# Kernel optimization log

Hardware: AMD Instinct MI355X
Metric: run time of the kernel (lower is better)

Reference implementation:

```python
import jax, jax.numpy as jnp
import numpy as np

N_NODES = 50000

def _gat_layer(x, src, dst, W, a_l, a_r, bias, alpha, agg, act, n_nodes):
    # x: [N, in]; W: [in, H*F]; a_l, a_r: [H, F]; bias: [H*F]
    H, F = a_l.shape
    z = (x @ W).reshape(n_nodes, H, F)                      # [N,H,F]
    el = jnp.einsum('nhf,hf->nh', z, a_l)                   # [N,H]
    er = jnp.einsum('nhf,hf->nh', z, a_r)                   # [N,H]
    e = jax.nn.leaky_relu(el[src] + er[dst], alpha)         # [E,H]
    # segment softmax over in-edges of each destination node
    m = jax.ops.segment_max(e, dst, num_segments=n_nodes)   # [N,H]
    ex = jnp.exp(e - m[dst])                                # [E,H]
    s = jax.ops.segment_sum(ex, dst, num_segments=n_nodes)  # [N,H]
    attn = ex / jnp.maximum(s[dst], 1e-9)                   # [E,H]
    msg = attn[:, :, None] * z[src]                         # [E,H,F]
    h = jax.ops.segment_sum(msg, dst, num_segments=n_nodes) # [N,H,F]
    # identity residual (in_feats == H*F) as in DGL GATConv
    h = h + x.reshape(n_nodes, -1, F)
    h = h + bias.reshape(1, H, F)
    if agg == 'flatten':
        h = h.reshape(n_nodes, H * F)
    else:  # mean over heads
        h = h.mean(axis=1)
    if act is not None:
        h = act(h)
    return h


def setup_inputs() -> dict:
    key = jax.random.key(0)
    ks = jax.random.split(key, 14)
    N, E, D = N_NODES, 800000, 128
    H, F = 4, 32
    sc_in = 1.0 / np.sqrt(D)
    sc_h = 1.0 / np.sqrt(H * F)
    inp = {
        'feats': jax.random.normal(ks[0], (N, D), jnp.float32),
        'src': jax.random.randint(ks[1], (E,), 0, N),
        'dst': jax.random.randint(ks[2], (E,), 0, N),
        'W1': jax.random.normal(ks[3], (D, H * F), jnp.float32) * sc_in,
        'al1': jax.random.normal(ks[4], (H, F), jnp.float32) * sc_h,
        'ar1': jax.random.normal(ks[5], (H, F), jnp.float32) * sc_h,
        'b1': jnp.zeros((H * F,), jnp.float32),
        'W2': jax.random.normal(ks[6], (H * F, H * F), jnp.float32) * sc_h,
        'al2': jax.random.normal(ks[7], (H, F), jnp.float32) * sc_h,
        'ar2': jax.random.normal(ks[8], (H, F), jnp.float32) * sc_h,
        'b2': jnp.zeros((H * F,), jnp.float32),
        'Wp': jax.random.normal(ks[9], (F, 1), jnp.float32) / np.sqrt(F),
        'bp': jnp.zeros((1,), jnp.float32),
    }
    return inp


def reference(feats, src, dst, W1, al1, ar1, b1, W2, al2, ar2, b2, Wp, bp):
    h = _gat_layer(feats, src, dst, W1, al1, ar1, b1, 0.2, 'flatten', jax.nn.elu, N_NODES)
    h = _gat_layer(h, src, dst, W2, al2, ar2, b2, 0.2, 'mean', None, N_NODES)
    return h @ Wp + bp  # [N, 1]
```

## Files before the change

### kernel.cpp

```cpp
#include <hip/hip_runtime.h>
#include <hip/hip_bf16.h>

#define NN 50000
#define NE 800000
#define HF 128
#define MAXDEG 64

#define OFF_FLAG   0u
#define OFF_Z      16668672u
#define OFF_H1     29468672u
#define OFF_EL     42268672u
#define OFF_ER     43068672u
#define OFF_FILL   54000128u
#define OFF_ADJ2   60000000u

typedef __hip_bfloat16 bf16;
typedef unsigned short us16;

#define SCAT_B 3125
#define GEMM_B 782

typedef __attribute__((ext_vector_type(8))) short bf16x8;
typedef __attribute__((ext_vector_type(4))) float f32x4;

__device__ __forceinline__ float us2f(us16 u) {
  union { unsigned int i; float f; } c; c.i = ((unsigned int)u) << 16; return c.f;
}
__device__ __forceinline__ us16 f2us(float f) {
  bf16 h = __float2bfloat16(f);
  union { bf16 h; us16 u; } c; c.h = h; return c.u;
}
__device__ __forceinline__ float blo(unsigned v) {
  union { unsigned i; float f; } c; c.i = v << 16; return c.f;
}
__device__ __forceinline__ float bhi(unsigned v) {
  union { unsigned i; float f; } c; c.i = v & 0xffff0000u; return c.f;
}
__device__ __forceinline__ unsigned pk2(float a, float b) {
  return (unsigned)f2us(a) | ((unsigned)f2us(b) << 16);
}

__device__ __forceinline__ int detect_f32(const us16* __restrict__ u) {
  int t = threadIdx.x;
  int mx = 0;
  for (int i = t; i < 2048; i += 256) {
    int e = (u[i] >> 7) & 0xFF;
    mx = mx > e ? mx : e;
  }
#pragma unroll
  for (int m = 32; m >= 1; m >>= 1) {
    int o = __shfl_xor(mx, m);
    mx = mx > o ? mx : o;
  }
  __shared__ int sred[4];
  if ((t & 63) == 0) sred[t >> 6] = mx;
  __syncthreads();
  int a = sred[0] > sred[1] ? sred[0] : sred[1];
  int b = sred[2] > sred[3] ? sred[2] : sred[3];
  int r = a > b ? a : b;
  return r >= 135;
}

__global__ __launch_bounds__(256) void k_scatter(
    const int* __restrict__ src, const int* __restrict__ dst,
    int* __restrict__ fill, us16* __restrict__ adj2) {
  int e = blockIdx.x * 256 + threadIdx.x;
  int d = dst[e];
  int r = atomicAdd(&fill[d], 1);
  if (r < MAXDEG) adj2[(d << 6) + r] = (us16)src[e];
}

template <int LAYER>
__global__ __launch_bounds__(256) void k_gemm(
    const void* __restrict__ Xv, const void* __restrict__ Wv,
    const void* __restrict__ alr, const void* __restrict__ arr,
    us16* __restrict__ Z, float* __restrict__ el, float* __restrict__ er,
    int* __restrict__ flagp) {
  int tid = threadIdx.x;
  int bx = (int)blockIdx.x;

  __shared__ us16 Wl[HF * HF];
  int f;
  if (LAYER == 1) {
    f = detect_f32((const us16*)Wv);
    if (bx == 0 && tid == 0) *flagp = f;
  } else {
    f = *flagp;
  }

  {
    const float* Wf = (const float*)Wv;
    const us16* Wb = (const us16*)Wv;
    for (int e = tid; e < HF * HF; e += 256) {
      int k = e >> 7, n = e & 127;
      int d = ((((k >> 5) * 8 + (n >> 4)) * 4 + ((k >> 3) & 3)) * 16 + (n & 15)) * 8 + (k & 7);
      Wl[d] = f ? f2us(Wf[e]) : Wb[e];
    }
  }
  __syncthreads();

  int w = tid >> 6;
  int lane = tid & 63;
  int q = lane >> 4;
  int c = lane & 15;
  int m0 = bx * 64 + w * 16;

  int rA = m0 + c;
  if (rA >= NN) rA = NN - 1;
  const us16* xb = (const us16*)Xv + (size_t)rA * HF;
  const float* xf = (const float*)Xv + (size_t)rA * HF;

  f32x4 acc[8] = {};
#pragma unroll
  for (int s = 0; s < 4; ++s) {
    bf16x8 a;
    if (LAYER == 1 && f) {
      float4 v0 = *(const float4*)&xf[s * 32 + q * 8];
      float4 v1 = *(const float4*)&xf[s * 32 + q * 8 + 4];
      union { us16 u[8]; bf16x8 v; } cv;
      cv.u[0] = f2us(v0.x); cv.u[1] = f2us(v0.y);
      cv.u[2] = f2us(v0.z); cv.u[3] = f2us(v0.w);
      cv.u[4] = f2us(v1.x); cv.u[5] = f2us(v1.y);
      cv.u[6] = f2us(v1.z); cv.u[7] = f2us(v1.w);
      a = cv.v;
    } else {
      a = *(const bf16x8*)&xb[s * 32 + q * 8];
    }
#pragma unroll
    for (int t = 0; t < 8; ++t) {
      bf16x8 bb = *(const bf16x8*)&Wl[((((s * 8) + t) * 4 + q) * 16 + c) * 8];
      acc[t] = __builtin_amdgcn_mfma_f32_16x16x32_bf16(a, bb, acc[t], 0, 0, 0);
    }
  }

#pragma unroll
  for (int reg = 0; reg < 4; ++reg) {
    int row = m0 + q * 4 + reg;
    if (row < NN) {
      us16* zrow = Z + (size_t)row * HF;
#pragma unroll
      for (int t = 0; t < 8; ++t) zrow[t * 16 + c] = f2us(acc[t][reg]);
    }
  }

  float alv[8], arv[8];
  {
    const float* alf = (const float*)alr; const us16* alb = (const us16*)alr;
    const float* arf = (const float*)arr; const us16* arb = (const us16*)arr;
#pragma unroll
    for (int t = 0; t < 8; ++t) {
      alv[t] = f ? alf[t * 16 + c] : us2f(alb[t * 16 + c]);
      arv[t] = f ? arf[t * 16 + c] : us2f(arb[t * 16 + c]);
    }
  }
#pragma unroll
  for (int reg = 0; reg < 4; ++reg) {
    int row = m0 + q * 4 + reg;
    float pl[4], pr[4];
#pragma unroll
    for (int h = 0; h < 4; ++h) {
      pl[h] = acc[2 * h][reg] * alv[2 * h] + acc[2 * h + 1][reg] * alv[2 * h + 1];
      pr[h] = acc[2 * h][reg] * arv[2 * h] + acc[2 * h + 1][reg] * arv[2 * h + 1];
    }
#pragma unroll
    for (int m = 1; m < 16; m <<= 1) {
#pragma unroll
      for (int h = 0; h < 4; ++h) {
        pl[h] += __shfl_xor(pl[h], m);
        pr[h] += __shfl_xor(pr[h], m);
      }
    }
    if (row < NN) {
      int cc = c & 3;
      float vl = cc == 0 ? pl[0] : cc == 1 ? pl[1] : cc == 2 ? pl[2] : pl[3];
      float vr = cc == 0 ? pr[0] : cc == 1 ? pr[1] : cc == 2 ? pr[2] : pr[3];
      if (c < 4) el[row * 4 + cc] = vl;
      else if (c < 8) er[row * 4 + cc] = vr;
    }
  }
}

template <int LAYER>
__global__ __launch_bounds__(256) void k_agg(
    const us16* __restrict__ Z, const float* __restrict__ el,
    const float* __restrict__ er, const int* __restrict__ fill,
    const us16* __restrict__ adj2, const void* __restrict__ resid,
    const void* __restrict__ bias, us16* __restrict__ Hout,
    const void* __restrict__ Wp, const void* __restrict__ bp,
    void* __restrict__ out, const int* __restrict__ flag) {
  int f = *flag;
  int n = blockIdx.x * 4 + (threadIdx.x >> 6);
  int lane = threadIdx.x & 63;
  int g = lane >> 4;
  int p = lane & 15;
  int hl = p >> 2;
  int f0 = p * 8;
  int begin = n << 6;

  int sl = (int)adj2[begin + lane];

  int deg = fill[n];
  if (deg > MAXDEG) deg = MAXDEG;
  float erh = er[n * 4 + hl];

  float acc[8] = {};
  float ssum = 0.f;
  for (int k = 0; k * 8 < deg; ++k) {
    int i0 = g + k * 8;
    int i1 = i0 + 4;
    int s0 = __shfl(sl, i0);
    int s1 = __shfl(sl, i1);
    bool v0 = i0 < deg;
    bool v1 = i1 < deg;
    s0 = v0 ? s0 : 0;
    s1 = v1 ? s1 : 0;
    float l0 = el[s0 * 4 + hl];
    float l1 = el[s1 * 4 + hl];
    uint4 za = *(const uint4*)&Z[(size_t)s0 * HF + f0];
    uint4 zb = *(const uint4*)&Z[(size_t)s1 * HF + f0];
    float sc0 = l0 + erh; sc0 = sc0 > 0.f ? sc0 : 0.2f * sc0;
    float sc1 = l1 + erh; sc1 = sc1 > 0.f ? sc1 : 0.2f * sc1;
    float ex0 = v0 ? __expf(sc0) : 0.f;
    float ex1 = v1 ? __expf(sc1) : 0.f;
    ssum += ex0 + ex1;
    acc[0] = fmaf(ex0, blo(za.x), acc[0]); acc[1] = fmaf(ex0, bhi(za.x), acc[1]);
    acc[2] = fmaf(ex0, blo(za.y), acc[2]); acc[3] = fmaf(ex0, bhi(za.y), acc[3]);
    acc[4] = fmaf(ex0, blo(za.z), acc[4]); acc[5] = fmaf(ex0, bhi(za.z), acc[5]);
    acc[6] = fmaf(ex0, blo(za.w), acc[6]); acc[7] = fmaf(ex0, bhi(za.w), acc[7]);
    acc[0] = fmaf(ex1, blo(zb.x), acc[0]); acc[1] = fmaf(ex1, bhi(zb.x), acc[1]);
    acc[2] = fmaf(ex1, blo(zb.y), acc[2]); acc[3] = fmaf(ex1, bhi(zb.y), acc[3]);
    acc[4] = fmaf(ex1, blo(zb.z), acc[4]); acc[5] = fmaf(ex1, bhi(zb.z), acc[5]);
    acc[6] = fmaf(ex1, blo(zb.w), acc[6]); acc[7] = fmaf(ex1, bhi(zb.w), acc[7]);
  }
  ssum += __shfl_xor(ssum, 16); ssum += __shfl_xor(ssum, 32);
#pragma unroll
  for (int j = 0; j < 8; ++j) {
    acc[j] += __shfl_xor(acc[j], 16);
    acc[j] += __shfl_xor(acc[j], 32);
  }
  float inv = 1.f / fmaxf(ssum, 1e-9f);

  float rx[8];
  if (LAYER == 1 && f) {
    const float* rf = (const float*)resid + (size_t)n * HF + f0;
    float4 r0 = *(const float4*)rf;
    float4 r1 = *(const float4*)(rf + 4);
    rx[0] = r0.x; rx[1] = r0.y; rx[2] = r0.z; rx[3] = r0.w;
    rx[4] = r1.x; rx[5] = r1.y; rx[6] = r1.z; rx[7] = r1.w;
  } else {
    uint4 xq = *(const uint4*)((const us16*)resid + (size_t)n * HF + f0);
    rx[0] = blo(xq.x); rx[1] = bhi(xq.x); rx[2] = blo(xq.y); rx[3] = bhi(xq.y);
    rx[4] = blo(xq.z); rx[5] = bhi(xq.z); rx[6] = blo(xq.w); rx[7] = bhi(xq.w);
  }
  float bv[8];
  if (f) {
    const float* bf_ = (const float*)bias + f0;
    bv[0] = bf_[0]; bv[1] = bf_[1]; bv[2] = bf_[2]; bv[3] = bf_[3];
    bv[4] = bf_[4]; bv[5] = bf_[5]; bv[6] = bf_[6]; bv[7] = bf_[7];
  } else {
    uint4 bq = *(const uint4*)((const us16*)bias + f0);
    bv[0] = blo(bq.x); bv[1] = bhi(bq.x); bv[2] = blo(bq.y); bv[3] = bhi(bq.y);
    bv[4] = blo(bq.z); bv[5] = bhi(bq.z); bv[6] = blo(bq.w); bv[7] = bhi(bq.w);
  }
  float t0 = fmaf(acc[0], inv, rx[0] + bv[0]);
  float t1 = fmaf(acc[1], inv, rx[1] + bv[1]);
  float t2 = fmaf(acc[2], inv, rx[2] + bv[2]);
  float t3 = fmaf(acc[3], inv, rx[3] + bv[3]);
  float t4 = fmaf(acc[4], inv, rx[4] + bv[4]);
  float t5 = fmaf(acc[5], inv, rx[5] + bv[5]);
  float t6 = fmaf(acc[6], inv, rx[6] + bv[6]);
  float t7 = fmaf(acc[7], inv, rx[7] + bv[7]);

  if (LAYER == 1) {
    t0 = t0 > 0.f ? t0 : __expf(t0) - 1.f;
    t1 = t1 > 0.f ? t1 : __expf(t1) - 1.f;
    t2 = t2 > 0.f ? t2 : __expf(t2) - 1.f;
    t3 = t3 > 0.f ? t3 : __expf(t3) - 1.f;
    t4 = t4 > 0.f ? t4 : __expf(t4) - 1.f;
    t5 = t5 > 0.f ? t5 : __expf(t5) - 1.f;
    t6 = t6 > 0.f ? t6 : __expf(t6) - 1.f;
    t7 = t7 > 0.f ? t7 : __expf(t7) - 1.f;
    if (g == 0) {
      uint4 o;
      o.x = pk2(t0, t1); o.y = pk2(t2, t3); o.z = pk2(t4, t5); o.w = pk2(t6, t7);
      *(uint4*)&Hout[(size_t)n * HF + f0] = o;
    }
  } else {
    t0 += __shfl_xor(t0, 4); t0 += __shfl_xor(t0, 8);
    t1 += __shfl_xor(t1, 4); t1 += __shfl_xor(t1, 8);
    t2 += __shfl_xor(t2, 4); t2 += __shfl_xor(t2, 8);
    t3 += __shfl_xor(t3, 4); t3 += __shfl_xor(t3, 8);
    t4 += __shfl_xor(t4, 4); t4 += __shfl_xor(t4, 8);
    t5 += __shfl_xor(t5, 4); t5 += __shfl_xor(t5, 8);
    t6 += __shfl_xor(t6, 4); t6 += __shfl_xor(t6, 8);
    t7 += __shfl_xor(t7, 4); t7 += __shfl_xor(t7, 8);
    int fw = (p & 3) * 8;
    float wv0, wv1, wv2, wv3, wv4, wv5, wv6, wv7;
    if (f) {
      const float* wpf = (const float*)Wp;
      wv0 = wpf[fw];     wv1 = wpf[fw + 1]; wv2 = wpf[fw + 2]; wv3 = wpf[fw + 3];
      wv4 = wpf[fw + 4]; wv5 = wpf[fw + 5]; wv6 = wpf[fw + 6]; wv7 = wpf[fw + 7];
    } else {
      const us16* wpb = (const us16*)Wp;
      wv0 = us2f(wpb[fw]);     wv1 = us2f(wpb[fw + 1]);
      wv2 = us2f(wpb[fw + 2]); wv3 = us2f(wpb[fw + 3]);
      wv4 = us2f(wpb[fw + 4]); wv5 = us2f(wpb[fw + 5]);
      wv6 = us2f(wpb[fw + 6]); wv7 = us2f(wpb[fw + 7]);
    }
    float pr = 0.25f * (t0 * wv0 + t1 * wv1 + t2 * wv2 + t3 * wv3 +
                        t4 * wv4 + t5 * wv5 + t6 * wv6 + t7 * wv7);
    pr += __shfl_xor(pr, 1); pr += __shfl_xor(pr, 2);
    if (lane == 0) {
      float bpv = f ? ((const float*)bp)[0] : us2f(((const us16*)bp)[0]);
      float res = pr + bpv;
      if (f) ((float*)out)[n] = res;
      else ((us16*)out)[n] = f2us(res);
    }
  }
}

extern "C" void kernel_launch(void* const* d_in, const int* in_sizes, int n_in,
                              void* d_out, int out_size, void* d_ws, size_t ws_size,
                              hipStream_t stream) {
  const int* src = (const int*)d_in[1];
  const int* dst = (const int*)d_in[2];
  char* ws = (char*)d_ws;
  int* flag   = (int*)(ws + OFF_FLAG);
  us16* z     = (us16*)(ws + OFF_Z);
  us16* h1    = (us16*)(ws + OFF_H1);
  float* el   = (float*)(ws + OFF_EL);
  float* er   = (float*)(ws + OFF_ER);
  int* fill   = (int*)(ws + OFF_FILL);
  us16* adj2  = (us16*)(ws + OFF_ADJ2);

  hipMemsetAsync(fill, 0, (size_t)NN * 4, stream);

  hipLaunchKernelGGL(k_scatter, dim3(SCAT_B), dim3(256), 0, stream,
                     src, dst, fill, adj2);
  hipLaunchKernelGGL((k_gemm<1>), dim3(GEMM_B), dim3(256), 0, stream,
                     d_in[0], d_in[3], d_in[4], d_in[5], z, el, er, flag);
  hipLaunchKernelGGL((k_agg<1>), dim3(NN / 4), dim3(256), 0, stream, z, el, er,
                     fill, adj2, d_in[0], d_in[6], h1,
                     (const void*)nullptr, (const void*)nullptr, (void*)nullptr, flag);
  hipLaunchKernelGGL((k_gemm<2>), dim3(GEMM_B), dim3(256), 0, stream,
                     h1, d_in[7], d_in[8], d_in[9], z, el, er, flag);
  hipLaunchKernelGGL((k_agg<2>), dim3(NN / 4), dim3(256), 0, stream, z, el, er,
                     fill, adj2, h1, d_in[10], (us16*)nullptr,
                     d_in[11], d_in[12], d_out, flag);
}
```

Measured before the change: 268.3 us.

## Pre-swizzle weights and params once in a fused scatter+prep kernel

Folds weight conversion/swizzling for both layers and the small parameter vectors into extra blocks of the edge-scatter kernel, writing bf16 copies to workspace. The GEMM kernels then drop the per-block LDS staging of W, the format detection and the syncthreads, and read pre-swizzled B fragments straight from global memory (cached in L2). The intent is to remove redundant per-block weight conversion work across 782 blocks in each GEMM. The cost is that B fragments now come from global/L2 rather than LDS, and bias, Wp and bp are rounded to bf16 even when the inputs are f32.

```diff
diff --git a/kernel.cpp b/kernel.cpp
--- a/kernel.cpp
+++ b/kernel.cpp
@@ -7,6 +7,9 @@
 #define MAXDEG 64
 
 #define OFF_FLAG   0u
+#define OFF_WC1    16601088u
+#define OFF_WC2    16633856u
+#define OFF_PAR    16666624u
 #define OFF_Z      16668672u
 #define OFF_H1     29468672u
 #define OFF_EL     42268672u
@@ -17,7 +20,9 @@
 typedef __hip_bfloat16 bf16;
 typedef unsigned short us16;
 
+#define PREP_B 132
 #define SCAT_B 3125
+#define SP_GRID (PREP_B + SCAT_B)
 #define GEMM_B 782
 
 typedef __attribute__((ext_vector_type(8))) short bf16x8;
@@ -61,44 +66,64 @@
   return r >= 135;
 }
 
-__global__ __launch_bounds__(256) void k_scatter(
+__global__ __launch_bounds__(256) void k_scat_prep(
     const int* __restrict__ src, const int* __restrict__ dst,
-    int* __restrict__ fill, us16* __restrict__ adj2) {
-  int e = blockIdx.x * 256 + threadIdx.x;
-  int d = dst[e];
-  int r = atomicAdd(&fill[d], 1);
-  if (r < MAXDEG) adj2[(d << 6) + r] = (us16)src[e];
+    int* __restrict__ fill, us16* __restrict__ adj2,
+    const void* __restrict__ W1r, const void* __restrict__ W2r,
+    const void* s2, const void* s3, const void* s4, const void* s5,
+    const void* s6, const void* s7, const void* s8, const void* s9,
+    us16* __restrict__ wc1, us16* __restrict__ wc2,
+    us16* d2, us16* d3, us16* d4, us16* d5, us16* d6, us16* d7,
+    us16* d8, us16* d9, int* __restrict__ flagp) {
+  int b = (int)blockIdx.x;
+  int t = threadIdx.x;
+  if (b >= PREP_B) {
+    int e = (b - PREP_B) * 256 + t;
+    int d = dst[e];
+    int r = atomicAdd(&fill[d], 1);
+    if (r < MAXDEG) adj2[(d << 6) + r] = (us16)src[e];
+    return;
+  }
+  int f = detect_f32((const us16*)W1r);
+  if (b == 0 && t == 0) *flagp = f;
+  if (b < 128) {
+    const void* Wr = b < 64 ? W1r : W2r;
+    us16* wc = b < 64 ? wc1 : wc2;
+    int e = (b & 63) * 256 + t;
+    int k = e >> 7, n = e & 127;
+    int d = ((((k >> 5) * 8 + (n >> 4)) * 4 + ((k >> 3) & 3)) * 16 + (n & 15)) * 8 + (k & 7);
+    us16 v;
+    if (f) v = f2us(((const float*)Wr)[e]);
+    else v = ((const us16*)Wr)[e];
+    wc[d] = v;
+  } else {
+    const void* sp[8] = {s2, s3, s4, s5, s6, s7, s8, s9};
+    us16* dp[8] = {d2, d3, d4, d5, d6, d7, d8, d9};
+    const int cnt[8] = {128, 128, 128, 128, 128, 128, 32, 1};
+    int gid = (b - 128) * 256 + t;
+    int base = 0;
+#pragma unroll
+    for (int p = 0; p < 8; ++p) {
+      int loc = gid - base;
+      if (loc >= 0 && loc < cnt[p]) {
+        us16 v;
+        if (f) v = f2us(((const float*)sp[p])[loc]);
+        else v = ((const us16*)sp[p])[loc];
+        dp[p][loc] = v;
+      }
+      base += cnt[p];
+    }
+  }
 }
 
 template <int LAYER>
 __global__ __launch_bounds__(256) void k_gemm(
-    const void* __restrict__ Xv, const void* __restrict__ Wv,
-    const void* __restrict__ alr, const void* __restrict__ arr,
+    const void* __restrict__ Xv, const us16* __restrict__ Wc,
+    const us16* __restrict__ al, const us16* __restrict__ ar,
     us16* __restrict__ Z, float* __restrict__ el, float* __restrict__ er,
-    int* __restrict__ flagp) {
+    const int* __restrict__ flagp) {
   int tid = threadIdx.x;
   int bx = (int)blockIdx.x;
-
-  __shared__ us16 Wl[HF * HF];
-  int f;
-  if (LAYER == 1) {
-    f = detect_f32((const us16*)Wv);
-    if (bx == 0 && tid == 0) *flagp = f;
-  } else {
-    f = *flagp;
-  }
-
-  {
-    const float* Wf = (const float*)Wv;
-    const us16* Wb = (const us16*)Wv;
-    for (int e = tid; e < HF * HF; e += 256) {
-      int k = e >> 7, n = e & 127;
-      int d = ((((k >> 5) * 8 + (n >> 4)) * 4 + ((k >> 3) & 3)) * 16 + (n & 15)) * 8 + (k & 7);
-      Wl[d] = f ? f2us(Wf[e]) : Wb[e];
-    }
-  }
-  __syncthreads();
-
   int w = tid >> 6;
   int lane = tid & 63;
   int q = lane >> 4;
@@ -110,11 +135,10 @@
   const us16* xb = (const us16*)Xv + (size_t)rA * HF;
   const float* xf = (const float*)Xv + (size_t)rA * HF;
 
-  f32x4 acc[8] = {};
-#pragma unroll
-  for (int s = 0; s < 4; ++s) {
-    bf16x8 a;
-    if (LAYER == 1 && f) {
+  bf16x8 afr[4];
+  if (LAYER == 1 && *flagp) {
+#pragma unroll
+    for (int s = 0; s < 4; ++s) {
       float4 v0 = *(const float4*)&xf[s * 32 + q * 8];
       float4 v1 = *(const float4*)&xf[s * 32 + q * 8 + 4];
       union { us16 u[8]; bf16x8 v; } cv;
@@ -122,14 +146,20 @@
       cv.u[2] = f2us(v0.z); cv.u[3] = f2us(v0.w);
       cv.u[4] = f2us(v1.x); cv.u[5] = f2us(v1.y);
       cv.u[6] = f2us(v1.z); cv.u[7] = f2us(v1.w);
-      a = cv.v;
-    } else {
-      a = *(const bf16x8*)&xb[s * 32 + q * 8];
-    }
+      afr[s] = cv.v;
+    }
+  } else {
+#pragma unroll
+    for (int s = 0; s < 4; ++s) afr[s] = *(const bf16x8*)&xb[s * 32 + q * 8];
+  }
+
+  f32x4 acc[8] = {};
+#pragma unroll 1
+  for (int s = 0; s < 4; ++s) {
 #pragma unroll
     for (int t = 0; t < 8; ++t) {
-      bf16x8 bb = *(const bf16x8*)&Wl[((((s * 8) + t) * 4 + q) * 16 + c) * 8];
-      acc[t] = __builtin_amdgcn_mfma_f32_16x16x32_bf16(a, bb, acc[t], 0, 0, 0);
+      bf16x8 bb = *(const bf16x8*)&Wc[(size_t)((s * 8 + t) * 64 + lane) * 8];
+      acc[t] = __builtin_amdgcn_mfma_f32_16x16x32_bf16(afr[s], bb, acc[t], 0, 0, 0);
     }
   }
 
@@ -144,14 +174,10 @@
   }
 
   float alv[8], arv[8];
-  {
-    const float* alf = (const float*)alr; const us16* alb = (const us16*)alr;
-    const float* arf = (const float*)arr; const us16* arb = (const us16*)arr;
-#pragma unroll
-    for (int t = 0; t < 8; ++t) {
-      alv[t] = f ? alf[t * 16 + c] : us2f(alb[t * 16 + c]);
-      arv[t] = f ? arf[t * 16 + c] : us2f(arb[t * 16 + c]);
-    }
+#pragma unroll
+  for (int t = 0; t < 8; ++t) {
+    alv[t] = us2f(al[t * 16 + c]);
+    arv[t] = us2f(ar[t * 16 + c]);
   }
 #pragma unroll
   for (int reg = 0; reg < 4; ++reg) {
@@ -185,8 +211,8 @@
     const us16* __restrict__ Z, const float* __restrict__ el,
     const float* __restrict__ er, const int* __restrict__ fill,
     const us16* __restrict__ adj2, const void* __restrict__ resid,
-    const void* __restrict__ bias, us16* __restrict__ Hout,
-    const void* __restrict__ Wp, const void* __restrict__ bp,
+    const us16* __restrict__ bias, us16* __restrict__ Hout,
+    const us16* __restrict__ Wp, const us16* __restrict__ bp,
     void* __restrict__ out, const int* __restrict__ flag) {
   int f = *flag;
   int n = blockIdx.x * 4 + (threadIdx.x >> 6);
@@ -252,24 +278,15 @@
     rx[0] = blo(xq.x); rx[1] = bhi(xq.x); rx[2] = blo(xq.y); rx[3] = bhi(xq.y);
     rx[4] = blo(xq.z); rx[5] = bhi(xq.z); rx[6] = blo(xq.w); rx[7] = bhi(xq.w);
   }
-  float bv[8];
-  if (f) {
-    const float* bf_ = (const float*)bias + f0;
-    bv[0] = bf_[0]; bv[1] = bf_[1]; bv[2] = bf_[2]; bv[3] = bf_[3];
-    bv[4] = bf_[4]; bv[5] = bf_[5]; bv[6] = bf_[6]; bv[7] = bf_[7];
-  } else {
-    uint4 bq = *(const uint4*)((const us16*)bias + f0);
-    bv[0] = blo(bq.x); bv[1] = bhi(bq.x); bv[2] = blo(bq.y); bv[3] = bhi(bq.y);
-    bv[4] = blo(bq.z); bv[5] = bhi(bq.z); bv[6] = blo(bq.w); bv[7] = bhi(bq.w);
-  }
-  float t0 = fmaf(acc[0], inv, rx[0] + bv[0]);
-  float t1 = fmaf(acc[1], inv, rx[1] + bv[1]);
-  float t2 = fmaf(acc[2], inv, rx[2] + bv[2]);
-  float t3 = fmaf(acc[3], inv, rx[3] + bv[3]);
-  float t4 = fmaf(acc[4], inv, rx[4] + bv[4]);
-  float t5 = fmaf(acc[5], inv, rx[5] + bv[5]);
-  float t6 = fmaf(acc[6], inv, rx[6] + bv[6]);
-  float t7 = fmaf(acc[7], inv, rx[7] + bv[7]);
+  uint4 bq = *(const uint4*)&bias[f0];
+  float t0 = fmaf(acc[0], inv, rx[0] + blo(bq.x));
+  float t1 = fmaf(acc[1], inv, rx[1] + bhi(bq.x));
+  float t2 = fmaf(acc[2], inv, rx[2] + blo(bq.y));
+  float t3 = fmaf(acc[3], inv, rx[3] + bhi(bq.y));
+  float t4 = fmaf(acc[4], inv, rx[4] + blo(bq.z));
+  float t5 = fmaf(acc[5], inv, rx[5] + bhi(bq.z));
+  float t6 = fmaf(acc[6], inv, rx[6] + blo(bq.w));
+  float t7 = fmaf(acc[7], inv, rx[7] + bhi(bq.w));
 
   if (LAYER == 1) {
     t0 = t0 > 0.f ? t0 : __expf(t0) - 1.f;
@@ -295,24 +312,13 @@
     t6 += __shfl_xor(t6, 4); t6 += __shfl_xor(t6, 8);
     t7 += __shfl_xor(t7, 4); t7 += __shfl_xor(t7, 8);
     int fw = (p & 3) * 8;
-    float wv0, wv1, wv2, wv3, wv4, wv5, wv6, wv7;
-    if (f) {
-      const float* wpf = (const float*)Wp;
-      wv0 = wpf[fw];     wv1 = wpf[fw + 1]; wv2 = wpf[fw + 2]; wv3 = wpf[fw + 3];
-      wv4 = wpf[fw + 4]; wv5 = wpf[fw + 5]; wv6 = wpf[fw + 6]; wv7 = wpf[fw + 7];
-    } else {
-      const us16* wpb = (const us16*)Wp;
-      wv0 = us2f(wpb[fw]);     wv1 = us2f(wpb[fw + 1]);
-      wv2 = us2f(wpb[fw + 2]); wv3 = us2f(wpb[fw + 3]);
-      wv4 = us2f(wpb[fw + 4]); wv5 = us2f(wpb[fw + 5]);
-      wv6 = us2f(wpb[fw + 6]); wv7 = us2f(wpb[fw + 7]);
-    }
-    float pr = 0.25f * (t0 * wv0 + t1 * wv1 + t2 * wv2 + t3 * wv3 +
-                        t4 * wv4 + t5 * wv5 + t6 * wv6 + t7 * wv7);
+    float pr = 0.25f * (t0 * us2f(Wp[fw]) + t1 * us2f(Wp[fw + 1]) +
+                        t2 * us2f(Wp[fw + 2]) + t3 * us2f(Wp[fw + 3]) +
+                        t4 * us2f(Wp[fw + 4]) + t5 * us2f(Wp[fw + 5]) +
+                        t6 * us2f(Wp[fw + 6]) + t7 * us2f(Wp[fw + 7]));
     pr += __shfl_xor(pr, 1); pr += __shfl_xor(pr, 2);
     if (lane == 0) {
-      float bpv = f ? ((const float*)bp)[0] : us2f(((const us16*)bp)[0]);
-      float res = pr + bpv;
+      float res = pr + us2f(bp[0]);
       if (f) ((float*)out)[n] = res;
       else ((us16*)out)[n] = f2us(res);
     }
@@ -326,6 +332,16 @@
   const int* dst = (const int*)d_in[2];
   char* ws = (char*)d_ws;
   int* flag   = (int*)(ws + OFF_FLAG);
+  us16* wc1   = (us16*)(ws + OFF_WC1);
+  us16* wc2   = (us16*)(ws + OFF_WC2);
+  us16* al1   = (us16*)(ws + OFF_PAR + 0);
+  us16* ar1   = (us16*)(ws + OFF_PAR + 256);
+  us16* b1    = (us16*)(ws + OFF_PAR + 512);
+  us16* al2   = (us16*)(ws + OFF_PAR + 768);
+  us16* ar2   = (us16*)(ws + OFF_PAR + 1024);
+  us16* b2    = (us16*)(ws + OFF_PAR + 1280);
+  us16* wp    = (us16*)(ws + OFF_PAR + 1536);
+  us16* bp    = (us16*)(ws + OFF_PAR + 1792);
   us16* z     = (us16*)(ws + OFF_Z);
   us16* h1    = (us16*)(ws + OFF_H1);
   float* el   = (float*)(ws + OFF_EL);
@@ -335,16 +351,19 @@
 
   hipMemsetAsync(fill, 0, (size_t)NN * 4, stream);
 
-  hipLaunchKernelGGL(k_scatter, dim3(SCAT_B), dim3(256), 0, stream,
-                     src, dst, fill, adj2);
+  hipLaunchKernelGGL(k_scat_prep, dim3(SP_GRID), dim3(256), 0, stream,
+                     src, dst, fill, adj2,
+                     d_in[3], d_in[7], d_in[4], d_in[5], d_in[6],
+                     d_in[8], d_in[9], d_in[10], d_in[11], d_in[12],
+                     wc1, wc2, al1, ar1, b1, al2, ar2, b2, wp, bp, flag);
   hipLaunchKernelGGL((k_gemm<1>), dim3(GEMM_B), dim3(256), 0, stream,
-                     d_in[0], d_in[3], d_in[4], d_in[5], z, el, er, flag);
+                     d_in[0], wc1, al1, ar1, z, el, er, flag);
   hipLaunchKernelGGL((k_agg<1>), dim3(NN / 4), dim3(256), 0, stream, z, el, er,
-                     fill, adj2, d_in[0], d_in[6], h1,
-                     (const void*)nullptr, (const void*)nullptr, (void*)nullptr, flag);
+                     fill, adj2, d_in[0], b1, h1,
+                     (const us16*)nullptr, (const us16*)nullptr, (void*)nullptr, flag);
   hipLaunchKernelGGL((k_gemm<2>), dim3(GEMM_B), dim3(256), 0, stream,
-                     h1, d_in[7], d_in[8], d_in[9], z, el, er, flag);
+                     h1, wc2, al2, ar2, z, el, er, flag);
   hipLaunchKernelGGL((k_agg<2>), dim3(NN / 4), dim3(256), 0, stream, z, el, er,
-                     fill, adj2, h1, d_in[10], (us16*)nullptr,
-                     d_in[11], d_in[12], d_out, flag);
-}
+                     fill, adj2, h1, b2, (us16*)nullptr,
+                     wp, bp, d_out, flag);
+}
```

Measured after the change: 277.9 us. 1.04x slower.
